# Kernel tuning notes

Measured on AMD Instinct MI355X. Metric: run time of the kernel, lower is better.

The kernel has to match this reference:

```python
import jax, jax.numpy as jnp
import numpy as np

INNER_DIM = 64
NUM_LABELS = 16
BIG_NEG = 1e12


def setup_inputs() -> dict:
    key = jax.random.key(0)
    k1, k2 = jax.random.split(key)
    B, S, H = 8, 512, 768
    sequence_output = jax.random.normal(k1, (B, S, H), dtype=jnp.float32)
    attention_mask = jnp.ones((B, S), dtype=jnp.int32)
    W = jax.random.normal(k2, (NUM_LABELS * INNER_DIM * 2, H), dtype=jnp.float32) * 0.02
    b = jnp.zeros((NUM_LABELS * INNER_DIM * 2,), dtype=jnp.float32)
    return {"sequence_output": sequence_output, "attention_mask": attention_mask,
            "W": W, "b": b}


def _rope_sincos(seq_len, dim, dtype):
    # interleaved sinusoidal embedding: [sin0,cos0,sin1,cos1,...]
    pos = jnp.arange(seq_len, dtype=dtype)[:, None]              # [S,1]
    idx = jnp.arange(dim // 2, dtype=dtype)
    theta = jnp.power(jnp.asarray(1000.0, dtype), -2.0 * idx / dim)
    ang = pos * theta                                            # [S, dim/2]
    # cos_pos/sin_pos after repeat_interleave(2): [c0,c0,c1,c1,...]
    cos_pos = jnp.repeat(jnp.cos(ang), 2, axis=-1)               # [S, dim]
    sin_pos = jnp.repeat(jnp.sin(ang), 2, axis=-1)               # [S, dim]
    return sin_pos, cos_pos


def _rotate_half_interleaved(x):
    # stack([-x[...,1::2], x[...,::2]], -1).reshape(x.shape)
    x2 = jnp.stack([-x[..., 1::2], x[..., ::2]], axis=-1)
    return x2.reshape(x.shape)


def reference(sequence_output, attention_mask, W, b):
    B, S, H = sequence_output.shape
    L, D = NUM_LABELS, INNER_DIM
    # dense projection then split into per-label q/k: [B,S,L,2D]
    out = (sequence_output @ W.T + b).reshape(B, S, L, 2 * D)
    qw, kw = out[..., :D], out[..., D:]                          # [B,S,L,D]

    sin_pos, cos_pos = _rope_sincos(S, D, sequence_output.dtype)
    cos_pos = cos_pos[None, :, None, :]                          # [1,S,1,D]
    sin_pos = sin_pos[None, :, None, :]
    qw = qw * cos_pos + _rotate_half_interleaved(qw) * sin_pos
    kw = kw * cos_pos + _rotate_half_interleaved(kw) * sin_pos

    logits = jnp.einsum('bmhd,bnhd->bhmn', qw, kw)               # [B,L,S,S]

    pad = attention_mask.astype(logits.dtype)[:, None, None, :]  # [B,1,1,S]
    logits = logits * pad - (1.0 - pad) * BIG_NEG

    tril = jnp.tril(jnp.ones((S, S), dtype=logits.dtype), -1)    # strictly lower
    logits = logits - tril * BIG_NEG
    return logits / (D ** 0.5)
```

## Files before the change

kernel.cpp:

```cpp
#include <hip/hip_runtime.h>
#include <hip/hip_bf16.h>

typedef __bf16 bf16;
typedef __attribute__((ext_vector_type(8))) __bf16 bf16x8;
typedef __attribute__((ext_vector_type(4))) float f32x4;
typedef __attribute__((ext_vector_type(4))) int i32x4;
typedef __attribute__((ext_vector_type(2))) unsigned int u32x2;
typedef __attribute__((ext_vector_type(4))) unsigned int u32x4;

#define BIG_NEG 1000000000000.0f
#define NEG_LOG_STEP 0.21586735253866545f
#define EXP_NEG_STEP 0.8058421877614818f

#define GLOAD_LDS16(g, l)                                                     \
    __builtin_amdgcn_global_load_lds(                                         \
        (const __attribute__((address_space(1))) void*)(g),                   \
        (__attribute__((address_space(3))) void*)(l), 16, 0, 0)

static __device__ inline u32x2 pack4_bf16(f32x4 v) {
    union { bf16 h[4]; u32x2 u; } t;
    t.h[0] = (bf16)v.x; t.h[1] = (bf16)v.y; t.h[2] = (bf16)v.z; t.h[3] = (bf16)v.w;
    return t.u;
}

__global__ __launch_bounds__(256) void convert_kernel(
    const float* __restrict__ X, const float* __restrict__ W,
    bf16* __restrict__ Xb, bf16* __restrict__ Wb)
{
    const int NX8 = (8 * 512 * 768) / 8;
    int idx = blockIdx.x * 256 + threadIdx.x;
    const float* src; bf16* dst; int i;
    if (idx < NX8) { src = X; dst = Xb; i = idx; }
    else           { src = W; dst = Wb; i = idx - NX8; }
    f32x4 a = __builtin_nontemporal_load(reinterpret_cast<const f32x4*>(src) + i * 2);
    f32x4 b = __builtin_nontemporal_load(reinterpret_cast<const f32x4*>(src) + i * 2 + 1);
    u32x2 lo = pack4_bf16(a), hi = pack4_bf16(b);
    u32x4 o; o.x = lo.x; o.y = lo.y; o.z = hi.x; o.w = hi.y;
    reinterpret_cast<u32x4*>(dst)[i] = o;
}

__global__ __launch_bounds__(256) void proj_rope_kernel(
    const bf16* __restrict__ A, const bf16* __restrict__ B,
    const float* __restrict__ bias,
    bf16* __restrict__ q_ws, bf16* __restrict__ k_ws)
{
    const int K = 768;
    __shared__ __align__(16) bf16 As[128][32];
    __shared__ __align__(16) bf16 Bs[128][32];

    const int tid  = threadIdx.x;
    const int lane = tid & 63;
    const int wave = tid >> 6;
    const int wr   = wave >> 1;
    const int wc   = wave & 1;
    const int brow = blockIdx.x * 128;
    const int bcol = blockIdx.y * 128;
    const int lane15 = lane & 15;
    const int kq = (lane >> 4) * 8;
    const int srow = lane >> 2;
    const int scol = (lane & 3) * 8;

    f32x4 acc[4][4] = {};

    for (int k0 = 0; k0 < K; k0 += 32) {
        #pragma unroll
        for (int p = 0; p < 2; ++p) {
            int r0 = p * 64 + wave * 16;
            GLOAD_LDS16(A + (size_t)(brow + r0 + srow) * K + k0 + scol, &As[r0][0]);
            GLOAD_LDS16(B + (size_t)(bcol + r0 + srow) * K + k0 + scol, &Bs[r0][0]);
        }
        __syncthreads();

        bf16x8 af[4], bfv[4];
        #pragma unroll
        for (int mf = 0; mf < 4; ++mf)
            af[mf] = *reinterpret_cast<bf16x8*>(&As[wr * 64 + mf * 16 + lane15][kq]);
        #pragma unroll
        for (int nf = 0; nf < 4; ++nf)
            bfv[nf] = *reinterpret_cast<bf16x8*>(&Bs[wc * 64 + nf * 16 + lane15][kq]);
        #pragma unroll
        for (int nf = 0; nf < 4; ++nf)
            #pragma unroll
            for (int mf = 0; mf < 4; ++mf)
                acc[nf][mf] = __builtin_amdgcn_mfma_f32_16x16x32_bf16(
                    bfv[nf], af[mf], acc[nf][mf], 0, 0, 0);
        __syncthreads();
    }

    const int mb = brow + wr * 64 + lane15;
    const int nb = bcol + wc * 64 + (lane >> 4) * 4;
    #pragma unroll
    for (int nf = 0; nf < 4; ++nf) {
        int n0 = nb + nf * 16;
        int d0 = n0 & 127;
        int l  = n0 >> 7;
        int dd = d0 & 63;
        int p0 = dd >> 1;
        float th0 = __expf(-(float)p0 * NEG_LOG_STEP);
        float th1 = th0 * EXP_NEG_STEP;
        f32x4 bn = *reinterpret_cast<const f32x4*>(&bias[n0]);
        bf16* dst = (d0 < 64) ? q_ws : k_ws;
        #pragma unroll
        for (int mf = 0; mf < 4; ++mf) {
            int m = mb + mf * 16;
            int s = m & 511;
            int b = m >> 9;
            float fs = (float)s;
            f32x4 a = acc[nf][mf];
            float v0 = a.x + bn.x, v1 = a.y + bn.y;
            float v2 = a.z + bn.z, v3 = a.w + bn.w;
            float sn0, cs0, sn1, cs1;
            __sincosf(fs * th0, &sn0, &cs0);
            __sincosf(fs * th1, &sn1, &cs1);
            union { bf16 h[4]; u32x2 u; } t;
            t.h[0] = (bf16)(v0 * cs0 - v1 * sn0);
            t.h[1] = (bf16)(v1 * cs0 + v0 * sn0);
            t.h[2] = (bf16)(v2 * cs1 - v3 * sn1);
            t.h[3] = (bf16)(v3 * cs1 + v2 * sn1);
            *reinterpret_cast<u32x2*>(
                &dst[(((size_t)(b * 16 + l) * 512) + s) * 64 + dd]) = t.u;
        }
    }
}

__global__ __launch_bounds__(256) void attn_kernel(
    const bf16* __restrict__ q_ws, const bf16* __restrict__ k_ws,
    const int* __restrict__ mask, float* __restrict__ out)
{
    const int tid  = threadIdx.x;
    const int lane = tid & 63;
    const int wave = tid >> 6;
    const int wr   = wave >> 1;
    const int wc   = wave & 1;
    const int bl   = blockIdx.z;
    const int brow = blockIdx.x * 128;
    const int bcol = blockIdx.y * 128;
    const int b    = bl >> 4;
    const int* mrow = mask + b * 512;
    float* obase = out + (size_t)bl * 512 * 512;

    if (brow >= bcol + 128) {
        int cg = tid & 31;
        int n0 = bcol + cg * 4;
        i32x4 mi = *reinterpret_cast<const i32x4*>(&mrow[n0]);
        f32x4 o;
        o.x = (-(1.0f - (float)mi.x) * BIG_NEG - BIG_NEG) * 0.125f;
        o.y = (-(1.0f - (float)mi.y) * BIG_NEG - BIG_NEG) * 0.125f;
        o.z = (-(1.0f - (float)mi.z) * BIG_NEG - BIG_NEG) * 0.125f;
        o.w = (-(1.0f - (float)mi.w) * BIG_NEG - BIG_NEG) * 0.125f;
        int r0 = tid >> 5;
        #pragma unroll
        for (int i = 0; i < 16; ++i) {
            int row = brow + i * 8 + r0;
            __builtin_nontemporal_store(
                o, reinterpret_cast<f32x4*>(&obase[(size_t)row * 512 + n0]));
        }
        return;
    }

    const bf16* qbase = q_ws + (size_t)bl * 512 * 64;
    const bf16* kbase = k_ws + (size_t)bl * 512 * 64;
    const int lane15 = lane & 15;
    const int kq = (lane >> 4) * 8;

    f32x4 acc[4][4] = {};
    #pragma unroll
    for (int ks = 0; ks < 2; ++ks) {
        bf16x8 qf[4], kf[4];
        #pragma unroll
        for (int mf = 0; mf < 4; ++mf)
            qf[mf] = *reinterpret_cast<const bf16x8*>(
                &qbase[(size_t)(brow + wr * 64 + mf * 16 + lane15) * 64 + ks * 32 + kq]);
        #pragma unroll
        for (int nf = 0; nf < 4; ++nf)
            kf[nf] = *reinterpret_cast<const bf16x8*>(
                &kbase[(size_t)(bcol + wc * 64 + nf * 16 + lane15) * 64 + ks * 32 + kq]);
        #pragma unroll
        for (int nf = 0; nf < 4; ++nf)
            #pragma unroll
            for (int mf = 0; mf < 4; ++mf)
                acc[nf][mf] = __builtin_amdgcn_mfma_f32_16x16x32_bf16(
                    kf[nf], qf[mf], acc[nf][mf], 0, 0, 0);
    }

    const int nb = bcol + wc * 64 + (lane >> 4) * 4;
    const int mbase = brow + wr * 64 + lane15;
    #pragma unroll
    for (int nf = 0; nf < 4; ++nf) {
        int n0 = nb + nf * 16;
        i32x4 mi = *reinterpret_cast<const i32x4*>(&mrow[n0]);
        f32x4 pf; pf.x = (float)mi.x; pf.y = (float)mi.y;
        pf.z = (float)mi.z; pf.w = (float)mi.w;
        f32x4 mt;
        mt.x = (1.0f - pf.x) * BIG_NEG; mt.y = (1.0f - pf.y) * BIG_NEG;
        mt.z = (1.0f - pf.z) * BIG_NEG; mt.w = (1.0f - pf.w) * BIG_NEG;
        #pragma unroll
        for (int mf = 0; mf < 4; ++mf) {
            int m = mbase + mf * 16;
            f32x4 a = acc[nf][mf];
            f32x4 o;
            o.x = (a.x * pf.x - mt.x - ((m > n0 + 0) ? BIG_NEG : 0.0f)) * 0.125f;
            o.y = (a.y * pf.y - mt.y - ((m > n0 + 1) ? BIG_NEG : 0.0f)) * 0.125f;
            o.z = (a.z * pf.z - mt.z - ((m > n0 + 2) ? BIG_NEG : 0.0f)) * 0.125f;
            o.w = (a.w * pf.w - mt.w - ((m > n0 + 3) ? BIG_NEG : 0.0f)) * 0.125f;
            *reinterpret_cast<f32x4*>(&obase[(size_t)m * 512 + n0]) = o;
        }
    }
}

extern "C" void kernel_launch(void* const* d_in, const int* in_sizes, int n_in,
                              void* d_out, int out_size, void* d_ws, size_t ws_size,
                              hipStream_t stream) {
    const float* X    = (const float*)d_in[0];
    const int*   mask = (const int*)d_in[1];
    const float* W    = (const float*)d_in[2];
    const float* bias = (const float*)d_in[3];

    float* out = (float*)d_out;

    bf16* q_ws = (bf16*)d_ws;
    bf16* k_ws = q_ws + (size_t)8 * 16 * 512 * 64;

    bf16* Xb = (bf16*)d_out;
    bf16* Wb = Xb + (size_t)8 * 512 * 768;

    const int NX8 = (8 * 512 * 768) / 8;
    const int NW8 = (2048 * 768) / 8;
    convert_kernel<<<(NX8 + NW8) / 256, 256, 0, stream>>>(X, W, Xb, Wb);
    proj_rope_kernel<<<dim3(32, 16), 256, 0, stream>>>(Xb, Wb, bias, q_ws, k_ws);
    attn_kernel<<<dim3(4, 4, 128), 256, 0, stream>>>(q_ws, k_ws, mask, out);
}
```

Before: 73.03 us.

## Double-buffer LDS tiles in projection GEMM to overlap loads with MFMA

The projection GEMM main loop now uses two LDS buffers per operand and issues the global-to-LDS loads for the next K tile before computing on the current one. This cuts one barrier per iteration and lets memory latency overlap with MFMA work. It doubles LDS use per block, which may lower occupancy. The projection kernel is only one part of the total kernel time.

Result: slower. 75.18 us (+2.9%).

```diff
diff --git a/kernel.cpp b/kernel.cpp
--- a/kernel.cpp
+++ b/kernel.cpp
@@ -45,8 +45,9 @@
     bf16* __restrict__ q_ws, bf16* __restrict__ k_ws)
 {
     const int K = 768;
-    __shared__ __align__(16) bf16 As[128][32];
-    __shared__ __align__(16) bf16 Bs[128][32];
+    const int NT = 24;
+    __shared__ __align__(16) bf16 As[2][128][32];
+    __shared__ __align__(16) bf16 Bs[2][128][32];
 
     const int tid  = threadIdx.x;
     const int lane = tid & 63;
@@ -60,32 +61,51 @@
     const int srow = lane >> 2;
     const int scol = (lane & 3) * 8;
 
+    const bf16* Abase = A + (size_t)(brow + wave * 16 + srow) * K + scol;
+    const bf16* Bbase = B + (size_t)(bcol + wave * 16 + srow) * K + scol;
+
     f32x4 acc[4][4] = {};
 
-    for (int k0 = 0; k0 < K; k0 += 32) {
-        #pragma unroll
-        for (int p = 0; p < 2; ++p) {
-            int r0 = p * 64 + wave * 16;
-            GLOAD_LDS16(A + (size_t)(brow + r0 + srow) * K + k0 + scol, &As[r0][0]);
-            GLOAD_LDS16(B + (size_t)(bcol + r0 + srow) * K + k0 + scol, &Bs[r0][0]);
-        }
+#define STAGE(buf, t)                                                          \
+    do {                                                                       \
+        int k0_ = (t) * 32;                                                    \
+        GLOAD_LDS16(Abase + k0_,              &As[buf][wave * 16][0]);         \
+        GLOAD_LDS16(Bbase + k0_,              &Bs[buf][wave * 16][0]);         \
+        GLOAD_LDS16(Abase + (size_t)64 * K + k0_, &As[buf][64 + wave * 16][0]);\
+        GLOAD_LDS16(Bbase + (size_t)64 * K + k0_, &Bs[buf][64 + wave * 16][0]);\
+    } while (0)
+
+#define COMPUTE(buf)                                                           \
+    do {                                                                       \
+        bf16x8 af[4], bfv[4];                                                  \
+        _Pragma("unroll")                                                      \
+        for (int mf = 0; mf < 4; ++mf)                                         \
+            af[mf] = *reinterpret_cast<bf16x8*>(                               \
+                &As[buf][wr * 64 + mf * 16 + lane15][kq]);                     \
+        _Pragma("unroll")                                                      \
+        for (int nf = 0; nf < 4; ++nf)                                         \
+            bfv[nf] = *reinterpret_cast<bf16x8*>(                              \
+                &Bs[buf][wc * 64 + nf * 16 + lane15][kq]);                     \
+        _Pragma("unroll")                                                      \
+        for (int nf = 0; nf < 4; ++nf)                                         \
+            _Pragma("unroll")                                                  \
+            for (int mf = 0; mf < 4; ++mf)                                     \
+                acc[nf][mf] = __builtin_amdgcn_mfma_f32_16x16x32_bf16(         \
+                    bfv[nf], af[mf], acc[nf][mf], 0, 0, 0);                    \
+    } while (0)
+
+    STAGE(0, 0);
+    __syncthreads();
+    for (int t = 0; t < NT; t += 2) {
+        if (t + 1 < NT) STAGE(1, t + 1);
+        COMPUTE(0);
         __syncthreads();
-
-        bf16x8 af[4], bfv[4];
-        #pragma unroll
-        for (int mf = 0; mf < 4; ++mf)
-            af[mf] = *reinterpret_cast<bf16x8*>(&As[wr * 64 + mf * 16 + lane15][kq]);
-        #pragma unroll
-        for (int nf = 0; nf < 4; ++nf)
-            bfv[nf] = *reinterpret_cast<bf16x8*>(&Bs[wc * 64 + nf * 16 + lane15][kq]);
-        #pragma unroll
-        for (int nf = 0; nf < 4; ++nf)
-            #pragma unroll
-            for (int mf = 0; mf < 4; ++mf)
-                acc[nf][mf] = __builtin_amdgcn_mfma_f32_16x16x32_bf16(
-                    bfv[nf], af[mf], acc[nf][mf], 0, 0, 0);
+        if (t + 2 < NT) STAGE(0, t + 2);
+        COMPUTE(1);
         __syncthreads();
     }
+#undef STAGE
+#undef COMPUTE
 
     const int mb = brow + wr * 64 + lane15;
     const int nb = bcol + wc * 64 + (lane >> 4) * 4;
```
